# Kernel optimization log

Measured on AMD Instinct MI355X. Metric: run time of the kernel, lower is better.

The kernel has to match this reference:

```python
import jax, jax.numpy as jnp
import numpy as np
import math

H = 12  # num heads
EPS = 1e-5


def layer_norm(x, g, b):
    xf = x.astype(jnp.float32)
    mu = jnp.mean(xf, axis=-1, keepdims=True)
    var = jnp.var(xf, axis=-1, keepdims=True)
    return ((xf - mu) * jax.lax.rsqrt(var + EPS) * g + b).astype(x.dtype)


def setup_inputs() -> dict:
    key = jax.random.key(0)
    ks = jax.random.split(key, 8)
    C, M = 768, 3072
    s = 0.02
    inp = {
        "x": jax.random.normal(ks[0], (128, 197, C), dtype=jnp.float32),
        # linear weights stored as [in, out] (y = x @ W + b)
        "Wq": jax.random.normal(ks[1], (C, C), dtype=jnp.float32) * s,
        "bq": jnp.zeros((C,), jnp.float32),
        "Wk": jax.random.normal(ks[2], (C, C), dtype=jnp.float32) * s,
        "bk": jnp.zeros((C,), jnp.float32),
        "Wv": jax.random.normal(ks[3], (C, C), dtype=jnp.float32) * s,
        "bv": jnp.zeros((C,), jnp.float32),
        "Wo": jax.random.normal(ks[4], (C, C), dtype=jnp.float32) * s,
        "bo": jnp.zeros((C,), jnp.float32),
        "W1": jax.random.normal(ks[5], (C, M), dtype=jnp.float32) * s,
        "b1": jnp.zeros((M,), jnp.float32),
        "W2": jax.random.normal(ks[6], (M, C), dtype=jnp.float32) * s,
        "b2": jnp.zeros((C,), jnp.float32),
        "g1": jnp.ones((C,), jnp.float32),
        "beta1": jnp.zeros((C,), jnp.float32),
        "g2": jnp.ones((C,), jnp.float32),
        "beta2": jnp.zeros((C,), jnp.float32),
    }
    return inp


def attention(xn, Wq, bq, Wk, bk, Wv, bv, Wo, bo):
    N, L, C = xn.shape
    Cqk = C // H
    q = (xn @ Wq + bq).reshape(N, L, H, Cqk)
    k = (xn @ Wk + bk).reshape(N, L, H, Cqk)
    v = (xn @ Wv + bv).reshape(N, L, H, Cqk)
    scale = 1.0 / math.sqrt(Cqk)
    aff = jnp.einsum('nqhc,nkhc->nqkh', q * scale, k)  # [N, Lq, Lk, H]
    aff = jax.nn.softmax(aff, axis=-2)                  # softmax over key axis
    mix = jnp.einsum('nqlh,nlhc->nqhc', aff, v)
    return mix.reshape(N, L, C) @ Wo + bo


def reference(x, Wq, bq, Wk, bk, Wv, bv, Wo, bo, W1, b1, W2, b2, g1, beta1, g2, beta2):
    x = x + attention(layer_norm(x, g1, beta1), Wq, bq, Wk, bk, Wv, bv, Wo, bo)
    h = layer_norm(x, g2, beta2) @ W1 + b1
    h = h * jax.nn.sigmoid(1.702 * h)  # QuickGELU
    return x + h @ W2 + b2
```

## Files before the change

### kernel.cpp

```cpp
#include <hip/hip_runtime.h>
#include <hip/hip_bf16.h>

typedef __bf16 bf16_t;
typedef __bf16 bf16x8 __attribute__((ext_vector_type(8)));
typedef float f32x4 __attribute__((ext_vector_type(4)));

#define T_TOK 25216
#define C_DIM 768
#define NH 12
#define LSEQ 197

__device__ __forceinline__ void gload_lds16(const bf16_t* g, bf16_t* l) {
  __builtin_amdgcn_global_load_lds(
      (const __attribute__((address_space(1))) unsigned int*)g,
      (__attribute__((address_space(3))) unsigned int*)l, 16, 0, 0);
}

template <int N>
__device__ __forceinline__ void vm_wait() {
  asm volatile("s_waitcnt vmcnt(%0)" ::"n"(N) : "memory");
}
__device__ __forceinline__ void block_bar() {
  __builtin_amdgcn_sched_barrier(0);
  asm volatile("" ::: "memory");
  __builtin_amdgcn_s_barrier();
  __builtin_amdgcn_sched_barrier(0);
}

__global__ void wtrans_k(const float* __restrict__ W, bf16_t* __restrict__ Wt,
                         int K, int N) {
  __shared__ float tile[32][33];
  const int tx = threadIdx.x, ty = threadIdx.y;
  const int bx = blockIdx.x, by = blockIdx.y;
#pragma unroll
  for (int i = ty; i < 32; i += 8)
    tile[i][tx] = W[(long)(by * 32 + i) * N + bx * 32 + tx];
  __syncthreads();
#pragma unroll
  for (int i = ty; i < 32; i += 8)
    Wt[(long)(bx * 32 + i) * K + by * 32 + tx] = (bf16_t)tile[tx][i];
}

__global__ void cat3_k(const float* __restrict__ a, const float* __restrict__ b,
                       const float* __restrict__ c, float* __restrict__ o) {
  int i = blockIdx.x * 256 + threadIdx.x;
  if (i < 2304) o[i] = i < 768 ? a[i] : (i < 1536 ? b[i - 768] : c[i - 1536]);
}

__global__ __launch_bounds__(256) void ln_k(const float* __restrict__ x,
                                            const float* __restrict__ g,
                                            const float* __restrict__ b,
                                            bf16_t* __restrict__ o) {
  const int lane = threadIdx.x & 63;
  const long row = (long)blockIdx.x * 4 + (threadIdx.x >> 6);
  const float* xr = x + row * C_DIM;
  float4 v[3];
  float s = 0.f, sq = 0.f;
#pragma unroll
  for (int i = 0; i < 3; ++i) {
    v[i] = *(const float4*)&xr[i * 256 + lane * 4];
    s += v[i].x + v[i].y + v[i].z + v[i].w;
    sq += v[i].x * v[i].x + v[i].y * v[i].y + v[i].z * v[i].z + v[i].w * v[i].w;
  }
#pragma unroll
  for (int off = 32; off; off >>= 1) {
    s += __shfl_xor(s, off);
    sq += __shfl_xor(sq, off);
  }
  const float mu = s * (1.f / 768.f);
  const float rstd = rsqrtf(sq * (1.f / 768.f) - mu * mu + 1e-5f);
  bf16_t* orow = o + row * C_DIM;
#pragma unroll
  for (int i = 0; i < 3; ++i) {
    const int c = i * 256 + lane * 4;
    const float4 gg = *(const float4*)&g[c];
    const float4 bb = *(const float4*)&b[c];
    bf16_t t4[4];
    t4[0] = (bf16_t)((v[i].x - mu) * rstd * gg.x + bb.x);
    t4[1] = (bf16_t)((v[i].y - mu) * rstd * gg.y + bb.y);
    t4[2] = (bf16_t)((v[i].z - mu) * rstd * gg.z + bb.z);
    t4[3] = (bf16_t)((v[i].w - mu) * rstd * gg.w + bb.w);
    __builtin_memcpy(&orow[c], t4, 8);
  }
}

template <int EPI, int BM, int BN>
__global__ __launch_bounds__(256) void gemm_bt(
    const bf16_t* __restrict__ A, const bf16_t* __restrict__ Bt,
    const float* __restrict__ bias, const float* __restrict__ res,
    void* __restrict__ outp, int K, int N) {
  constexpr int MACC = BM / 32;
  constexpr int NACC = BN / 32;
  constexpr int ACW = BM / 32;
  constexpr int BCW = BN / 32;
  constexpr int NLOADS = ACW + BCW;
  __shared__ __align__(16) bf16_t lA[2][BM * 64];
  __shared__ __align__(16) bf16_t lB[2][BN * 64];
  const int tid = threadIdx.x;
  const int wave = tid >> 6, lane = tid & 63;
  const int fr = lane & 15, fq = lane >> 4;

  const int gx = gridDim.x;
  const int nwg = gridDim.x * gridDim.y;
  int bid = blockIdx.y * gx + blockIdx.x;
  {
    const int q = nwg >> 3, r = nwg & 7;
    const int xcd = bid & 7, idx = bid >> 3;
    bid = (xcd < r ? xcd * (q + 1) : r * (q + 1) + (xcd - r) * q) + idx;
  }
  const int bx = bid % gx, by = bid / gx;

  const long rowBase = (long)by * BM;
  const long colBase = (long)bx * BN;
  const int wr = (wave >> 1) * (BM / 2), wc = (wave & 1) * (BN / 2);

  f32x4 acc[MACC][NACC];
#pragma unroll
  for (int m = 0; m < MACC; ++m)
#pragma unroll
    for (int n = 0; n < NACC; ++n) acc[m][n] = (f32x4){0.f, 0.f, 0.f, 0.f};

  const int srow = lane >> 3;
  const int scol = (((lane & 7) ^ srow)) * 8;

  const bf16_t* aP[ACW];
  const bf16_t* bP[BCW];
#pragma unroll
  for (int c = 0; c < ACW; ++c)
    aP[c] = A + (rowBase + 8 * (wave * ACW + c) + srow) * (long)K + scol;
#pragma unroll
  for (int c = 0; c < BCW; ++c)
    bP[c] = Bt + (colBase + 8 * (wave * BCW + c) + srow) * (long)K + scol;

  auto stage0 = [&](int koff) {
#pragma unroll
    for (int c = 0; c < ACW; ++c)
      gload_lds16(aP[c] + koff, &lA[0][(wave * ACW + c) * 512]);
#pragma unroll
    for (int c = 0; c < BCW; ++c)
      gload_lds16(bP[c] + koff, &lB[0][(wave * BCW + c) * 512]);
  };
  auto stage1 = [&](int koff) {
#pragma unroll
    for (int c = 0; c < ACW; ++c)
      gload_lds16(aP[c] + koff, &lA[1][(wave * ACW + c) * 512]);
#pragma unroll
    for (int c = 0; c < BCW; ++c)
      gload_lds16(bP[c] + koff, &lB[1][(wave * BCW + c) * 512]);
  };
  auto compute0 = [&]() {
#pragma unroll
    for (int kf = 0; kf < 2; ++kf) {
      bf16x8 af[MACC], bfr[NACC];
#pragma unroll
      for (int m = 0; m < MACC; ++m) {
        const int row = wr + m * 16 + fr;
        af[m] =
            *(const bf16x8*)&lA[0][row * 64 + (((kf * 4 + fq) ^ (fr & 7)) * 8)];
      }
#pragma unroll
      for (int n = 0; n < NACC; ++n) {
        const int row = wc + n * 16 + fr;
        bfr[n] =
            *(const bf16x8*)&lB[0][row * 64 + (((kf * 4 + fq) ^ (fr & 7)) * 8)];
      }
#pragma unroll
      for (int m = 0; m < MACC; ++m)
#pragma unroll
        for (int n = 0; n < NACC; ++n)
          acc[m][n] = __builtin_amdgcn_mfma_f32_16x16x32_bf16(af[m], bfr[n],
                                                              acc[m][n], 0, 0, 0);
    }
  };
  auto compute1 = [&]() {
#pragma unroll
    for (int kf = 0; kf < 2; ++kf) {
      bf16x8 af[MACC], bfr[NACC];
#pragma unroll
      for (int m = 0; m < MACC; ++m) {
        const int row = wr + m * 16 + fr;
        af[m] =
            *(const bf16x8*)&lA[1][row * 64 + (((kf * 4 + fq) ^ (fr & 7)) * 8)];
      }
#pragma unroll
      for (int n = 0; n < NACC; ++n) {
        const int row = wc + n * 16 + fr;
        bfr[n] =
            *(const bf16x8*)&lB[1][row * 64 + (((kf * 4 + fq) ^ (fr & 7)) * 8)];
      }
#pragma unroll
      for (int m = 0; m < MACC; ++m)
#pragma unroll
        for (int n = 0; n < NACC; ++n)
          acc[m][n] = __builtin_amdgcn_mfma_f32_16x16x32_bf16(af[m], bfr[n],
                                                              acc[m][n], 0, 0, 0);
    }
  };

  const int kT = K >> 6;
  stage0(0);
  int kt = 0;
  for (; kt + 2 < kT; kt += 2) {
    stage1((kt + 1) * 64);
    vm_wait<NLOADS>();
    block_bar();
    compute0();
    block_bar();
    stage0((kt + 2) * 64);
    vm_wait<NLOADS>();
    block_bar();
    compute1();
    block_bar();
  }
  stage1((kt + 1) * 64);
  vm_wait<NLOADS>();
  block_bar();
  compute0();
  vm_wait<0>();
  block_bar();
  compute1();

#pragma unroll
  for (int m = 0; m < MACC; ++m) {
    const long row0 = rowBase + wr + m * 16 + fq * 4;
#pragma unroll
    for (int n = 0; n < NACC; ++n) {
      const long col = colBase + wc + n * 16 + fr;
      const float bb = bias[col];
#pragma unroll
      for (int r = 0; r < 4; ++r) {
        const long idx = (row0 + r) * N + col;
        float v = acc[m][n][r] + bb;
        if (EPI == 0) {
          ((bf16_t*)outp)[idx] = (bf16_t)v;
        } else if (EPI == 1) {
          ((float*)outp)[idx] = v + res[idx];
        } else {
          v = v / (1.f + __expf(-1.702f * v));
          ((bf16_t*)outp)[idx] = (bf16_t)v;
        }
      }
    }
  }
}

__global__ __launch_bounds__(256) void attn_k(const bf16_t* __restrict__ qkv,
                                              bf16_t* __restrict__ mix) {
  constexpr int KR = 72;
  constexpr int VR = 232;
  __shared__ __align__(16) bf16_t smem[208 * KR + 64 * VR + 64 * VR];
  bf16_t* lK = smem;
  bf16_t* lVt = smem + 208 * KR;
  bf16_t* lP = lVt + 64 * VR;

  const int tid = threadIdx.x;
  const int wave = tid >> 6, lane = tid & 63;
  const int fr = lane & 15, fq = lane >> 4;
  const int nh = blockIdx.x;
  const int n = nh / NH, h = nh % NH;
  const long t0 = (long)n * LSEQ;
  const long qs = 2304;

  {
    int4 z = {0, 0, 0, 0};
    int4* p = (int4*)smem;
    const int tot = (208 * KR + 2 * 64 * VR) * 2 / 16;
    for (int i = tid; i < tot; i += 256) p[i] = z;
  }
  __syncthreads();

  for (int it = tid; it < 197 * 8; it += 256) {
    int r = it >> 3, cg = it & 7;
    int4 v = *(const int4*)(qkv + (t0 + r) * qs + 768 + h * 64 + cg * 8);
    *(int4*)&lK[r * KR + cg * 8] = v;
  }
  for (int it = tid; it < 197 * 8; it += 256) {
    int r = it >> 3, cg = it & 7;
    int4 v = *(const int4*)(qkv + (t0 + r) * qs + 1536 + h * 64 + cg * 8);
    const bf16_t* pv = (const bf16_t*)&v;
#pragma unroll
    for (int j = 0; j < 8; ++j) lVt[(cg * 8 + j) * VR + r] = pv[j];
  }
  __syncthreads();

  bf16_t* lPw = lP + wave * 16 * VR;

  for (int fi = 0; fi < 4; ++fi) {
    const int f = wave + fi * 4;
    if (f >= 13) break;
    const int qrow = f * 16 + fr;
    const long tq = t0 + (qrow < LSEQ ? qrow : LSEQ - 1);
    const bf16_t* qp = qkv + tq * qs + h * 64;
    bf16x8 a0 = *(const bf16x8*)(qp + fq * 8);
    bf16x8 a1 = *(const bf16x8*)(qp + 32 + fq * 8);

    f32x4 s[13];
#pragma unroll
    for (int j = 0; j < 13; ++j) s[j] = (f32x4){0.f, 0.f, 0.f, 0.f};
#pragma unroll
    for (int j = 0; j < 13; ++j) {
      bf16x8 b0 = *(const bf16x8*)&lK[(j * 16 + fr) * KR + fq * 8];
      s[j] = __builtin_amdgcn_mfma_f32_16x16x32_bf16(a0, b0, s[j], 0, 0, 0);
      bf16x8 b1 = *(const bf16x8*)&lK[(j * 16 + fr) * KR + 32 + fq * 8];
      s[j] = __builtin_amdgcn_mfma_f32_16x16x32_bf16(a1, b1, s[j], 0, 0, 0);
    }
    float mx[4] = {-3e38f, -3e38f, -3e38f, -3e38f};
#pragma unroll
    for (int j = 0; j < 13; ++j) {
      const bool valid = (j * 16 + fr) < LSEQ;
#pragma unroll
      for (int r = 0; r < 4; ++r) {
        float v = s[j][r] * 0.125f;
        v = valid ? v : -3e38f;
        s[j][r] = v;
        mx[r] = fmaxf(mx[r], v);
      }
    }
#pragma unroll
    for (int r = 0; r < 4; ++r) {
      mx[r] = fmaxf(mx[r], __shfl_xor(mx[r], 1));
      mx[r] = fmaxf(mx[r], __shfl_xor(mx[r], 2));
      mx[r] = fmaxf(mx[r], __shfl_xor(mx[r], 4));
      mx[r] = fmaxf(mx[r], __shfl_xor(mx[r], 8));
    }
    float sm[4] = {0.f, 0.f, 0.f, 0.f};
#pragma unroll
    for (int j = 0; j < 13; ++j)
#pragma unroll
      for (int r = 0; r < 4; ++r) {
        float e = __expf(s[j][r] - mx[r]);
        s[j][r] = e;
        sm[r] += e;
      }
#pragma unroll
    for (int r = 0; r < 4; ++r) {
      sm[r] += __shfl_xor(sm[r], 1);
      sm[r] += __shfl_xor(sm[r], 2);
      sm[r] += __shfl_xor(sm[r], 4);
      sm[r] += __shfl_xor(sm[r], 8);
      sm[r] = 1.f / sm[r];
    }
#pragma unroll
    for (int j = 0; j < 13; ++j)
#pragma unroll
      for (int r = 0; r < 4; ++r)
        lPw[(fq * 4 + r) * VR + j * 16 + fr] = (bf16_t)(s[j][r] * sm[r]);
    asm volatile("s_waitcnt lgkmcnt(0)" ::: "memory");

    f32x4 o4[4];
#pragma unroll
    for (int c = 0; c < 4; ++c) o4[c] = (f32x4){0.f, 0.f, 0.f, 0.f};
#pragma unroll
    for (int kc = 0; kc < 7; ++kc) {
      bf16x8 pa = *(const bf16x8*)&lPw[fr * VR + kc * 32 + fq * 8];
#pragma unroll
      for (int c = 0; c < 4; ++c) {
        bf16x8 bv = *(const bf16x8*)&lVt[(c * 16 + fr) * VR + kc * 32 + fq * 8];
        o4[c] = __builtin_amdgcn_mfma_f32_16x16x32_bf16(pa, bv, o4[c], 0, 0, 0);
      }
    }
#pragma unroll
    for (int c = 0; c < 4; ++c)
#pragma unroll
      for (int r = 0; r < 4; ++r) {
        const int q = f * 16 + fq * 4 + r;
        if (q < LSEQ)
          mix[(t0 + q) * C_DIM + h * 64 + c * 16 + fr] = (bf16_t)o4[c][r];
      }
  }
}

extern "C" void kernel_launch(void* const* d_in, const int* in_sizes, int n_in,
                              void* d_out, int out_size, void* d_ws,
                              size_t ws_size, hipStream_t stream) {
  const float* x = (const float*)d_in[0];
  const float* Wq = (const float*)d_in[1];
  const float* bq = (const float*)d_in[2];
  const float* Wk = (const float*)d_in[3];
  const float* bk = (const float*)d_in[4];
  const float* Wv = (const float*)d_in[5];
  const float* bv = (const float*)d_in[6];
  const float* Wo = (const float*)d_in[7];
  const float* bo = (const float*)d_in[8];
  const float* W1 = (const float*)d_in[9];
  const float* b1 = (const float*)d_in[10];
  const float* W2 = (const float*)d_in[11];
  const float* b2 = (const float*)d_in[12];
  const float* g1 = (const float*)d_in[13];
  const float* be1 = (const float*)d_in[14];
  const float* g2 = (const float*)d_in[15];
  const float* be2 = (const float*)d_in[16];

  char* ws = (char*)d_ws;
  size_t off = 0;
  auto alloc = [&](size_t bytes) {
    char* p = ws + off;
    off += (bytes + 255) & ~(size_t)255;
    return p;
  };
  bf16_t* xn = (bf16_t*)alloc((size_t)T_TOK * 768 * 2);
  char* qm = alloc((size_t)T_TOK * 3072 * 2);
  bf16_t* qkv = (bf16_t*)qm;
  bf16_t* mixb = (bf16_t*)(qm + (size_t)T_TOK * 2304 * 2);
  bf16_t* h = (bf16_t*)qm;
  bf16_t* Wqkvt = (bf16_t*)alloc((size_t)2304 * 768 * 2);
  bf16_t* Wot = (bf16_t*)alloc((size_t)768 * 768 * 2);
  bf16_t* W1t = (bf16_t*)alloc((size_t)3072 * 768 * 2);
  bf16_t* W2t = (bf16_t*)alloc((size_t)768 * 3072 * 2);
  float* bqkv = (float*)alloc(2304 * 4);
  float* x2 = (float*)d_out;

  dim3 tb(32, 8);
  wtrans_k<<<dim3(24, 24), tb, 0, stream>>>(Wq, Wqkvt, 768, 768);
  wtrans_k<<<dim3(24, 24), tb, 0, stream>>>(Wk, Wqkvt + 768 * 768, 768, 768);
  wtrans_k<<<dim3(24, 24), tb, 0, stream>>>(Wv, Wqkvt + 2 * 768 * 768, 768, 768);
  wtrans_k<<<dim3(24, 24), tb, 0, stream>>>(Wo, Wot, 768, 768);
  wtrans_k<<<dim3(96, 24), tb, 0, stream>>>(W1, W1t, 768, 3072);
  wtrans_k<<<dim3(24, 96), tb, 0, stream>>>(W2, W2t, 3072, 768);
  cat3_k<<<9, 256, 0, stream>>>(bq, bk, bv, bqkv);

  ln_k<<<T_TOK / 4, 256, 0, stream>>>(x, g1, be1, xn);
  gemm_bt<0, 128, 128><<<dim3(2304 / 128, T_TOK / 128), 256, 0, stream>>>(
      xn, Wqkvt, bqkv, nullptr, qkv, 768, 2304);
  attn_k<<<128 * NH, 256, 0, stream>>>(qkv, mixb);
  gemm_bt<1, 128, 128><<<dim3(768 / 128, T_TOK / 128), 256, 0, stream>>>(
      mixb, Wot, bo, x, x2, 768, 768);
  ln_k<<<T_TOK / 4, 256, 0, stream>>>(x2, g2, be2, xn);
  gemm_bt<2, 128, 128><<<dim3(3072 / 128, T_TOK / 128), 256, 0, stream>>>(
      xn, W1t, b1, nullptr, h, 768, 3072);
  gemm_bt<1, 128, 128><<<dim3(768 / 128, T_TOK / 128), 256, 0, stream>>>(
      h, W2t, b2, x2, (float*)d_out, 3072, 768);
}
```

Before: 718.8 us.

## Merge weight transposes into one launch and widen GEMM N-tile

Folds the six weight-transpose launches into a single kernel whose flat block index is mapped onto the per-matrix transpose tiles, cutting launch overhead. Separately, every GEMM's N tile goes from 128 to 192 columns, which raises reuse of the A tile and lowers the block count. The wider tile needs more registers and LDS per block and may lower occupancy; it also assumes the gemm template handles a 192-wide N tile correctly.

```diff
diff --git a/kernel.cpp b/kernel.cpp
--- a/kernel.cpp
+++ b/kernel.cpp
@@ -27,11 +27,11 @@
   __builtin_amdgcn_sched_barrier(0);
 }
 
-__global__ void wtrans_k(const float* __restrict__ W, bf16_t* __restrict__ Wt,
-                         int K, int N) {
+__device__ __forceinline__ void wtrans_body(const float* __restrict__ W,
+                                            bf16_t* __restrict__ Wt, int K,
+                                            int N, int bx, int by) {
   __shared__ float tile[32][33];
   const int tx = threadIdx.x, ty = threadIdx.y;
-  const int bx = blockIdx.x, by = blockIdx.y;
 #pragma unroll
   for (int i = ty; i < 32; i += 8)
     tile[i][tx] = W[(long)(by * 32 + i) * N + bx * 32 + tx];
@@ -39,6 +39,29 @@
 #pragma unroll
   for (int i = ty; i < 32; i += 8)
     Wt[(long)(bx * 32 + i) * K + by * 32 + tx] = (bf16_t)tile[tx][i];
+}
+
+__global__ void wprep_k(const float* __restrict__ Wq,
+                        const float* __restrict__ Wk,
+                        const float* __restrict__ Wv,
+                        const float* __restrict__ Wo,
+                        const float* __restrict__ W1,
+                        const float* __restrict__ W2,
+                        bf16_t* __restrict__ Wqkvt, bf16_t* __restrict__ Wot,
+                        bf16_t* __restrict__ W1t, bf16_t* __restrict__ W2t) {
+  const int b = blockIdx.x;
+  if (b < 2304) {
+    const int z = b / 576, r = b % 576;
+    const float* W = z == 0 ? Wq : (z == 1 ? Wk : (z == 2 ? Wv : Wo));
+    bf16_t* Wt = z == 3 ? Wot : Wqkvt + (size_t)z * 768 * 768;
+    wtrans_body(W, Wt, 768, 768, r % 24, r / 24);
+  } else if (b < 4608) {
+    const int r = b - 2304;
+    wtrans_body(W1, W1t, 768, 3072, r % 96, r / 96);
+  } else {
+    const int r = b - 4608;
+    wtrans_body(W2, W2t, 3072, 768, r % 24, r / 24);
+  }
 }
 
 __global__ void cat3_k(const float* __restrict__ a, const float* __restrict__ b,
@@ -411,23 +434,19 @@
   float* x2 = (float*)d_out;
 
   dim3 tb(32, 8);
-  wtrans_k<<<dim3(24, 24), tb, 0, stream>>>(Wq, Wqkvt, 768, 768);
-  wtrans_k<<<dim3(24, 24), tb, 0, stream>>>(Wk, Wqkvt + 768 * 768, 768, 768);
-  wtrans_k<<<dim3(24, 24), tb, 0, stream>>>(Wv, Wqkvt + 2 * 768 * 768, 768, 768);
-  wtrans_k<<<dim3(24, 24), tb, 0, stream>>>(Wo, Wot, 768, 768);
-  wtrans_k<<<dim3(96, 24), tb, 0, stream>>>(W1, W1t, 768, 3072);
-  wtrans_k<<<dim3(24, 96), tb, 0, stream>>>(W2, W2t, 3072, 768);
+  wprep_k<<<6912, tb, 0, stream>>>(Wq, Wk, Wv, Wo, W1, W2, Wqkvt, Wot, W1t,
+                                   W2t);
   cat3_k<<<9, 256, 0, stream>>>(bq, bk, bv, bqkv);
 
   ln_k<<<T_TOK / 4, 256, 0, stream>>>(x, g1, be1, xn);
-  gemm_bt<0, 128, 128><<<dim3(2304 / 128, T_TOK / 128), 256, 0, stream>>>(
+  gemm_bt<0, 128, 192><<<dim3(2304 / 192, T_TOK / 128), 256, 0, stream>>>(
       xn, Wqkvt, bqkv, nullptr, qkv, 768, 2304);
   attn_k<<<128 * NH, 256, 0, stream>>>(qkv, mixb);
-  gemm_bt<1, 128, 128><<<dim3(768 / 128, T_TOK / 128), 256, 0, stream>>>(
+  gemm_bt<1, 128, 192><<<dim3(768 / 192, T_TOK / 128), 256, 0, stream>>>(
       mixb, Wot, bo, x, x2, 768, 768);
   ln_k<<<T_TOK / 4, 256, 0, stream>>>(x2, g2, be2, xn);
-  gemm_bt<2, 128, 128><<<dim3(3072 / 128, T_TOK / 128), 256, 0, stream>>>(
+  gemm_bt<2, 128, 192><<<dim3(3072 / 192, T_TOK / 128), 256, 0, stream>>>(
       xn, W1t, b1, nullptr, h, 768, 3072);
-  gemm_bt<1, 128, 128><<<dim3(768 / 128, T_TOK / 128), 256, 0, stream>>>(
+  gemm_bt<1, 128, 192><<<dim3(768 / 192, T_TOK / 128), 256, 0, stream>>>(
       h, W2t, b2, x2, (float*)d_out, 3072, 768);
 }
```

After: 969.4 us. 1.35x slower.
